# Kernel optimization log

Hardware: AMD Instinct MI355X
Metric: run time of the kernel (lower is better)

## Reference

```python
import jax, jax.numpy as jnp
import numpy as np

B, L, D = 8, 2048, 128
K_CURV = 1.0  # Lorentz manifold curvature constant
NEG_INF = float(-2**32 + 1)


def _lorentz_linear(x, W, b, scale):
    # nn.Linear then project onto the Lorentz manifold (dropout is identity in eval).
    x = x @ W.T + b
    time = jax.nn.sigmoid(x[..., :1]) * jnp.exp(scale) + 1.1
    x_narrow = x[..., 1:]
    s = (time * time - K_CURV) / jnp.sum(x_narrow * x_narrow, axis=-1, keepdims=True)
    return jnp.concatenate([time, x_narrow * jnp.sqrt(s)], axis=-1)


def setup_inputs() -> dict:
    key = jax.random.key(0)
    ks = jax.random.split(key, 10)
    stdv = 0.02

    def lin_w(k):
        W = jax.random.uniform(k, (D, D), minval=-stdv, maxval=stdv, dtype=jnp.float32)
        return W.at[:, 0].set(0.0)  # reset_parameters zeros column 0

    inp = {
        'query': jax.random.normal(ks[0], (B, L, D), dtype=jnp.float32),
        'key': jax.random.normal(ks[1], (B, L, D), dtype=jnp.float32),
        'value': jax.random.normal(ks[2], (B, L, D), dtype=jnp.float32),
        'mask': jax.random.bernoulli(ks[3], 0.1, (B, L)),  # True = padded position
        'Wq': lin_w(ks[4]), 'bq': jnp.zeros((D,), jnp.float32), 'sq': jnp.asarray(2.3, jnp.float32),
        'Wk': lin_w(ks[5]), 'bk': jnp.zeros((D,), jnp.float32), 'sk': jnp.asarray(2.3, jnp.float32),
        'Wv': lin_w(ks[6]), 'bv': jnp.zeros((D,), jnp.float32), 'sv': jnp.asarray(2.3, jnp.float32),
        'attn_scale': jnp.asarray([np.sqrt(D)], jnp.float32),
        'attn_bias': jnp.asarray(0.0, jnp.float32),
    }
    return inp


def reference(query, key, value, mask, Wq, bq, sq, Wk, bk, sk, Wv, bv, sv, attn_scale, attn_bias):
    q = _lorentz_linear(query, Wq, bq, sq)  # [B, L, D]
    k = _lorentz_linear(key, Wk, bk, sk)
    v = _lorentz_linear(value, Wv, bv, sv)
    # single head: shape to [B, 1, L, D]
    q, k, v = q[:, None], k[:, None], v[:, None]

    # Lorentzian inner product: negate time component of q
    qk = jnp.einsum('bhqd,bhkd->bhqk', q.at[..., 0].multiply(-1.0), k)
    attn = (2.0 + 2.0 * qk) / attn_scale + attn_bias  # [B, 1, L, L]

    # pad mask [B, L] broadcast over query rows + causal (triu) mask
    pad = jnp.broadcast_to(mask[:, None, :], (B, L, L))
    tri = jnp.triu(jnp.ones((L, L), bool), k=1)
    m = (tri[None] | pad)[:, None]  # [B, 1, L, L]
    attn = jnp.where(m, NEG_INF, attn)
    attn = jax.nn.softmax(attn, axis=-1)

    # Lorentz mid-point: weighted sum, normalize by sqrt(|<ave, ave>_L|)
    ave = jnp.einsum('bhqk,bhkd->bhqd', attn, v)
    lor = -ave[..., :1] ** 2 + jnp.sum(ave[..., 1:] ** 2, axis=-1, keepdims=True)
    denom = jnp.sqrt(jnp.maximum(jnp.abs(-lor), 1e-8))
    out = jnp.sqrt(K_CURV) * ave / denom
    return out[:, 0]  # [B, L, D]
```

## Files before the change

### kernel.cpp

```cpp
#include <hip/hip_runtime.h>

typedef unsigned short u16;
typedef unsigned long long u64;
typedef __attribute__((ext_vector_type(8))) short short8;
typedef __attribute__((ext_vector_type(4))) float f32x4;

#define MFMA16(A,B,C) __builtin_amdgcn_mfma_f32_16x16x32_bf16(A,B,C,0,0,0)
#define NEG_INF_F (-4294967295.0f)

#define Bsz 8
#define Lsz 2048
#define Dsz 128

__device__ __forceinline__ u16 f2bf(float f){
  union { float f; unsigned u; } v; v.f = f;
  unsigned u = v.u;
  return (u16)((u + 0x7fffu + ((u >> 16) & 1u)) >> 16);
}
__device__ __forceinline__ float bf2f(u16 h){
  union { float f; unsigned u; } v; v.u = ((unsigned)h) << 16;
  return v.f;
}

__global__ __launch_bounds__(256) void wconv_kernel(
    const float* __restrict__ Wq, const float* __restrict__ Wk,
    const float* __restrict__ Wv, u16* __restrict__ wb)
{
  int i = blockIdx.x * 256 + threadIdx.x;
  if (i < 16384) wb[i] = f2bf(Wq[i]);
  else if (i < 32768) wb[i] = f2bf(Wk[i - 16384]);
  else if (i < 49152) wb[i] = f2bf(Wv[i - 32768]);
}

#define LPX 136
#define LPY 133

__global__ __launch_bounds__(256) void proj_kernel(
    const float* __restrict__ xq, const float* __restrict__ xk, const float* __restrict__ xv,
    const u16* __restrict__ wb,
    const float* __restrict__ bq, const float* __restrict__ bk, const float* __restrict__ bv,
    const float* __restrict__ sq, const float* __restrict__ sk, const float* __restrict__ sv,
    const float* __restrict__ attn_scale,
    u16* __restrict__ qout, u16* __restrict__ kout,
    u16* __restrict__ vthi, u16* __restrict__ vtlo,
    float* __restrict__ tqo, float* __restrict__ tko,
    float* __restrict__ vpart)
{
  const int z = blockIdx.z;
  const float* x  = (z == 0) ? xq : (z == 1) ? xk : xv;
  const u16*   Wb = wb + z * 16384;
  const float* bb = (z == 0) ? bq : (z == 1) ? bk : bv;
  const float* ss = (z == 0) ? sq : (z == 1) ? sk : sv;

  __shared__ u16  xl[64 * LPX];
  __shared__ u16  wl[128 * LPX];
  __shared__ float yl[64 * LPY];
  __shared__ float scl[64];
  __shared__ float tml[64];

  const int t = threadIdx.x;
  const long row0 = (long)blockIdx.x * 64;

  for (int i = t; i < 2048; i += 256) {
    int r = i >> 4, c8 = (i & 15) * 8;
    *(short8*)&wl[r * LPX + c8] = *(const short8*)&Wb[r * 128 + c8];
  }
  for (int i = t; i < 2048; i += 256) {
    int off = i * 4;
    int r = off >> 7, c = off & 127;
    f32x4 xv4 = *(const f32x4*)(x + row0 * 128 + off);
    u64 wv = (u64)f2bf(xv4[0]) | ((u64)f2bf(xv4[1]) << 16)
           | ((u64)f2bf(xv4[2]) << 32) | ((u64)f2bf(xv4[3]) << 48);
    *(u64*)&xl[r * LPX + c] = wv;
  }
  __syncthreads();

  const int l = t & 63, wid = t >> 6;
  const int qr = l & 15, g = l >> 4;
  const int r0 = wid * 16;

  short8 af[4];
#pragma unroll
  for (int ks = 0; ks < 4; ks++)
    af[ks] = *(const short8*)&xl[(r0 + qr) * LPX + ks * 32 + g * 8];

  f32x4 acc[8];
#pragma unroll
  for (int jt = 0; jt < 8; jt++) acc[jt] = (f32x4){0.f, 0.f, 0.f, 0.f};

#pragma unroll
  for (int ks = 0; ks < 4; ks++) {
#pragma unroll
    for (int jt = 0; jt < 8; jt++) {
      short8 bfr = *(const short8*)&wl[(jt * 16 + qr) * LPX + ks * 32 + g * 8];
      acc[jt] = MFMA16(af[ks], bfr, acc[jt]);
    }
  }

  float bbv[8];
#pragma unroll
  for (int jt = 0; jt < 8; jt++) bbv[jt] = bb[jt * 16 + qr];

  float ssq[4] = {0.f, 0.f, 0.f, 0.f};
#pragma unroll
  for (int jt = 0; jt < 8; jt++)
#pragma unroll
    for (int r = 0; r < 4; r++) {
      float yv = acc[jt][r] + bbv[jt];
      acc[jt][r] = yv;
      float s2 = yv * yv;
      if (jt == 0) s2 = (qr == 0) ? 0.f : s2;
      ssq[r] += s2;
    }
#pragma unroll
  for (int r = 0; r < 4; r++) {
    ssq[r] += __shfl_xor(ssq[r], 1);
    ssq[r] += __shfl_xor(ssq[r], 2);
    ssq[r] += __shfl_xor(ssq[r], 4);
    ssq[r] += __shfl_xor(ssq[r], 8);
  }

  const float es = __expf(ss[0]);
  const float fold = 2.0f / attn_scale[0];

  float tvv[4], sclv[4];
#pragma unroll
  for (int r = 0; r < 4; r++) {
    float y0 = __shfl(acc[0][r], l & 48);
    float tv = es / (1.0f + __expf(-y0)) + 1.1f;
    tvv[r] = tv;
    sclv[r] = sqrtf((tv * tv - 1.0f) / ssq[r]);
  }
  if (qr == 0) {
#pragma unroll
    for (int r = 0; r < 4; r++) {
      tml[r0 + g * 4 + r] = tvv[r];
      scl[r0 + g * 4 + r] = sclv[r];
    }
  }
#pragma unroll
  for (int jt = 0; jt < 8; jt++)
#pragma unroll
    for (int r = 0; r < 4; r++)
      yl[(r0 + g * 4 + r) * LPY + jt * 16 + qr] = acc[jt][r];
  __syncthreads();

  const long gbase = row0 * 128;
  if (z == 0) {
    for (int i = t; i < 64 * 128; i += 256) {
      int r = i >> 7, d = i & 127;
      float v = (d == 0) ? 0.f : yl[r * LPY + d] * scl[r] * fold;
      qout[gbase + i] = f2bf(v);
    }
    if (t < 64) tqo[row0 + t] = -tml[t] * fold;
  } else if (z == 1) {
    for (int i = t; i < 64 * 128; i += 256) {
      int r = i >> 7, d = i & 127;
      float v = (d == 0) ? 0.f : yl[r * LPY + d] * scl[r];
      kout[gbase + i] = f2bf(v);
    }
    if (t < 64) tko[row0 + t] = tml[t];
  } else {
    const int b = (int)(row0 >> 11);
    const int lpos = (int)(row0 & 2047);
    for (int i = t; i < 128 * 64; i += 256) {
      int d = i >> 6, r = i & 63;
      float v = (d == 0) ? tml[r] : yl[r * LPY + d] * scl[r];
      u16 hi = f2bf(v);
      float lo = v - bf2f(hi);
      long idx = ((long)(b * 128 + d)) * 2048 + lpos + r;
      vthi[idx] = hi;
      vtlo[idx] = f2bf(lo);
    }
    if (t < 128) {
      float s = 0.f;
      for (int r = 0; r < 64; r++)
        s += (t == 0) ? tml[r] : yl[r * LPY + t] * scl[r];
      int blk = (int)((row0 >> 6) & 31);
      vpart[((long)(b * 32 + blk)) * 128 + t] = s;
    }
  }
}

__global__ __launch_bounds__(256) void pack_mask_kernel(
    const int* __restrict__ mask, u64* __restrict__ pmask)
{
  int gt = blockIdx.x * 256 + threadIdx.x;
  int w = gt >> 6;
  int lane = gt & 63;
  if (w >= Bsz * 32) return;
  u64 word = __ballot(mask[w * 64 + lane] != 0);
  if (lane == 0) pmask[w] = word;
}

__global__ __launch_bounds__(128) void vreduce_kernel(
    const float* __restrict__ vpart, float* __restrict__ vsum)
{
  int i = blockIdx.x * 128 + threadIdx.x;
  int b = i >> 7, d = i & 127;
  float s = 0.f;
  for (int j = 0; j < 32; j++) s += vpart[((long)(b * 32 + j)) * 128 + d];
  vsum[i] = s;
}

__global__ __launch_bounds__(512, 2) void flash_kernel(
    const u16* __restrict__ qbf, const u16* __restrict__ kb,
    const u16* __restrict__ vthi, const u16* __restrict__ vtlo,
    const float* __restrict__ tq, const float* __restrict__ tk,
    const u64* __restrict__ pmask, const float* __restrict__ vsum,
    const float* __restrict__ sqp, const float* __restrict__ skp,
    const float* __restrict__ asp,
    float* __restrict__ out)
{
  __shared__ u16 Pl[2][32 * 128];
  __shared__ float lLd[8][2][16];
  __shared__ float ssqw[8][2][16];

  const int t = threadIdx.x;
  const int w = t >> 6, l = t & 63;
  const int qr = l & 15, g = l >> 4;
  const int blk = blockIdx.x;
  const int b = blk & 7;
  const int s = 63 - (blk >> 3);
  const int qbase = s * 32;
  const int nkt = (qbase + 159) >> 7;

  const float fold = 2.0f / asp[0];
  const float tqm = __expf(sqp[0]) + 1.1f;
  const float tkm = __expf(skp[0]) + 1.1f;
  const float MS = fold * sqrtf((tqm * tqm - 1.f) * (tkm * tkm - 1.f)) + 1.0f;

  short8 qf[2][4];
  float tqv0, tqv1;
  {
    const u16* qp0 = qbf + ((long)(b * 2048 + qbase + qr)) * 128 + g * 8;
    const u16* qp1 = qp0 + 16 * 128;
#pragma unroll
    for (int ks = 0; ks < 4; ks++) {
      qf[0][ks] = *(const short8*)(qp0 + ks * 32);
      qf[1][ks] = *(const short8*)(qp1 + ks * 32);
    }
    tqv0 = tq[b * 2048 + qbase + qr];
    tqv1 = tq[b * 2048 + qbase + 16 + qr];
  }

  const u16* kbase  = kb   + ((long)(b * 2048 + 16 * w + qr)) * 128 + g * 8;
  const u16* vhbase = vthi + ((long)(b * 128 + 16 * w + qr)) * 2048 + g * 8;
  const u16* vlbase = vtlo + ((long)(b * 128 + 16 * w + qr)) * 2048 + g * 8;

  float lsum0 = 0.f, lsum1 = 0.f;
  f32x4 acc0 = (f32x4){0.f, 0.f, 0.f, 0.f};
  f32x4 acc1 = (f32x4){0.f, 0.f, 0.f, 0.f};

  short8 kc[4], vh[4], vl[4];
#pragma unroll
  for (int ks = 0; ks < 4; ks++) kc[ks] = *(const short8*)(kbase + ks * 32);
  f32x4 tkvc = *(const f32x4*)(tk + b * 2048 + 16 * w + g * 4);
  u64 mwc = pmask[b * 32 + (w >> 2)];

  int cur = 0;
  for (int kt = 0; kt < nkt; kt++) {
    const long k0 = (long)kt << 7;

    f32x4 sv0 = (f32x4){0.f, 0.f, 0.f, 0.f};
    f32x4 sv1 = (f32x4){0.f, 0.f, 0.f, 0.f};
#pragma unroll
    for (int ks = 0; ks < 4; ks++) {
      sv0 = MFMA16(kc[ks], qf[0][ks], sv0);
      sv1 = MFMA16(kc[ks], qf[1][ks], sv1);
    }
    if (kt + 1 < nkt) {
      const u16* kp = kbase + (k0 + 128) * 128;
#pragma unroll
      for (int ks = 0; ks < 4; ks++) kc[ks] = *(const short8*)(kp + ks * 32);
    }

    const bool bndry = (k0 + 127 > qbase);
    float p0[4], p1[4];
#pragma unroll
    for (int r = 0; r < 4; r++) {
      int kl = 16 * w + 4 * g + r;
      bool bad = ((mwc >> (kl & 63)) & 1ull) != 0ull;
      bool bad0 = bad, bad1 = bad;
      if (bndry) {
        bad0 |= (k0 + kl > qbase + qr);
        bad1 |= (k0 + kl > qbase + 16 + qr);
      }
      float e0 = __expf(sv0[r] + tqv0 * tkvc[r] - MS);
      float e1 = __expf(sv1[r] + tqv1 * tkvc[r] - MS);
      p0[r] = bad0 ? 0.f : e0;
      p1[r] = bad1 ? 0.f : e1;
      lsum0 += p0[r];
      lsum1 += p1[r];
    }
    {
      int pch = ((2 * w + (g >> 1)) ^ (qr & 7)) * 8 + (g & 1) * 4;
      u64 w0 = (u64)f2bf(p0[0]) | ((u64)f2bf(p0[1]) << 16)
             | ((u64)f2bf(p0[2]) << 32) | ((u64)f2bf(p0[3]) << 48);
      u64 w1 = (u64)f2bf(p1[0]) | ((u64)f2bf(p1[1]) << 16)
             | ((u64)f2bf(p1[2]) << 32) | ((u64)f2bf(p1[3]) << 48);
      *(u64*)&Pl[cur][qr * 128 + pch] = w0;
      *(u64*)&Pl[cur][(16 + qr) * 128 + pch] = w1;
    }
    if (kt + 1 < nkt) {
      tkvc = *(const f32x4*)(tk + b * 2048 + k0 + 128 + 16 * w + g * 4);
      mwc = pmask[b * 32 + (int)(k0 >> 6) + 2 + (w >> 2)];
    }

    if (kt > 0) {
      const u16* Pb = &Pl[cur ^ 1][0];
#pragma unroll
      for (int ks = 0; ks < 4; ks++) {
        int ch = ((4 * ks + g) ^ (qr & 7)) * 8;
        short8 pf0 = *(const short8*)&Pb[qr * 128 + ch];
        short8 pf1 = *(const short8*)&Pb[(16 + qr) * 128 + ch];
        acc0 = MFMA16(vh[ks], pf0, acc0);
        acc0 = MFMA16(vl[ks], pf0, acc0);
        acc1 = MFMA16(vh[ks], pf1, acc1);
        acc1 = MFMA16(vl[ks], pf1, acc1);
      }
    }

#pragma unroll
    for (int ks = 0; ks < 4; ks++) {
      vh[ks] = *(const short8*)(vhbase + k0 + ks * 32);
      vl[ks] = *(const short8*)(vlbase + k0 + ks * 32);
    }

    asm volatile("s_waitcnt lgkmcnt(0)\n\ts_barrier" ::: "memory");
    cur ^= 1;
  }

  {
    const u16* Pb = &Pl[cur ^ 1][0];
#pragma unroll
    for (int ks = 0; ks < 4; ks++) {
      int ch = ((4 * ks + g) ^ (qr & 7)) * 8;
      short8 pf0 = *(const short8*)&Pb[qr * 128 + ch];
      short8 pf1 = *(const short8*)&Pb[(16 + qr) * 128 + ch];
      acc0 = MFMA16(vh[ks], pf0, acc0);
      acc0 = MFMA16(vl[ks], pf0, acc0);
      acc1 = MFMA16(vh[ks], pf1, acc1);
      acc1 = MFMA16(vl[ks], pf1, acc1);
    }
  }

  lsum0 += __shfl_xor(lsum0, 16); lsum0 += __shfl_xor(lsum0, 32);
  lsum1 += __shfl_xor(lsum1, 16); lsum1 += __shfl_xor(lsum1, 32);
  if (g == 0) { lLd[w][0][qr] = lsum0; lLd[w][1][qr] = lsum1; }
  __syncthreads();

  float Lt0 = 0.f, Lt1 = 0.f;
#pragma unroll
  for (int j = 0; j < 8; j++) { Lt0 += lLd[j][0][qr]; Lt1 += lLd[j][1][qr]; }
  const bool mrow0 = (Lt0 == 0.f);
  const bool mrow1 = (Lt1 == 0.f);
  const float invL0 = mrow0 ? 0.f : 1.0f / Lt0;
  const float invL1 = mrow1 ? 0.f : 1.0f / Lt1;

  const float* vs = vsum + b * 128;
  float av0[4], av1[4];
  float pp0 = 0.f, pp1 = 0.f;
#pragma unroll
  for (int r = 0; r < 4; r++) {
    int d = 16 * w + 4 * g + r;
    float u = vs[d] * (1.0f / 2048.0f);
    float a0 = mrow0 ? u : acc0[r] * invL0;
    float a1 = mrow1 ? u : acc1[r] * invL1;
    av0[r] = a0; av1[r] = a1;
    float sgn = (d == 0) ? -1.f : 1.f;
    pp0 += sgn * a0 * a0;
    pp1 += sgn * a1 * a1;
  }
  pp0 += __shfl_xor(pp0, 16); pp0 += __shfl_xor(pp0, 32);
  pp1 += __shfl_xor(pp1, 16); pp1 += __shfl_xor(pp1, 32);
  if (g == 0) { ssqw[w][0][qr] = pp0; ssqw[w][1][qr] = pp1; }
  __syncthreads();

  float lor0 = 0.f, lor1 = 0.f;
#pragma unroll
  for (int j = 0; j < 8; j++) { lor0 += ssqw[j][0][qr]; lor1 += ssqw[j][1][qr]; }
  float rd0 = 1.0f / sqrtf(fmaxf(fabsf(lor0), 1e-8f));
  float rd1 = 1.0f / sqrtf(fmaxf(fabsf(lor1), 1e-8f));

  float* op0 = out + ((long)(b * 2048 + qbase + qr)) * 128 + 16 * w + 4 * g;
  float* op1 = out + ((long)(b * 2048 + qbase + 16 + qr)) * 128 + 16 * w + 4 * g;
  f32x4 o0, o1;
  o0[0] = av0[0] * rd0; o0[1] = av0[1] * rd0; o0[2] = av0[2] * rd0; o0[3] = av0[3] * rd0;
  o1[0] = av1[0] * rd1; o1[1] = av1[1] * rd1; o1[2] = av1[2] * rd1; o1[3] = av1[3] * rd1;
  *(f32x4*)op0 = o0;
  *(f32x4*)op1 = o1;
}

extern "C" void kernel_launch(void* const* d_in, const int* in_sizes, int n_in,
                              void* d_out, int out_size, void* d_ws, size_t ws_size,
                              hipStream_t stream)
{
  const float* query = (const float*)d_in[0];
  const float* key   = (const float*)d_in[1];
  const float* value = (const float*)d_in[2];
  const int*   mask  = (const int*)d_in[3];
  const float* Wq = (const float*)d_in[4];
  const float* bq = (const float*)d_in[5];
  const float* sq = (const float*)d_in[6];
  const float* Wk = (const float*)d_in[7];
  const float* bk = (const float*)d_in[8];
  const float* sk = (const float*)d_in[9];
  const float* Wv = (const float*)d_in[10];
  const float* bv = (const float*)d_in[11];
  const float* sv = (const float*)d_in[12];
  const float* attn_scale = (const float*)d_in[13];

  float* out = (float*)d_out;
  char* ws = (char*)d_ws;

  float* vsum  = (float*)ws;
  u64*   pmask = (u64*)(ws + 4096);
  float* tqa   = (float*)(ws + 8192);
  float* tka   = (float*)(ws + 8192 + 65536);
  float* vpart = (float*)(ws + 8192 + 131072);
  u16*   wb    = (u16*)(ws + 8192 + 262144);
  char*  big   = ws + 8192 + 262144 + 131072;
  u16*   qbuf  = (u16*)big;
  u16*   kbuf  = qbuf + (size_t)16384 * 128;
  u16*   vthi  = kbuf + (size_t)16384 * 128;
  u16*   vtlo  = vthi + (size_t)16384 * 128;

  wconv_kernel<<<192, 256, 0, stream>>>(Wq, Wk, Wv, wb);
  proj_kernel<<<dim3(256, 1, 3), 256, 0, stream>>>(
      query, key, value, wb, bq, bk, bv, sq, sk, sv, attn_scale,
      qbuf, kbuf, vthi, vtlo, tqa, tka, vpart);
  pack_mask_kernel<<<64, 256, 0, stream>>>(mask, pmask);
  vreduce_kernel<<<8, 128, 0, stream>>>(vpart, vsum);
  flash_kernel<<<512, 512, 0, stream>>>(
      qbuf, kbuf, vthi, vtlo, tqa, tka, pmask, vsum, sq, sk, attn_scale, out);
}
```

Baseline: 101.7 us.

## Enlarge flash query tile to 64 rows and fuse small prep kernels

The flash kernel now handles 64 query rows per block instead of 32, so each K and V fragment loaded from global memory feeds four MFMA row groups rather than two, and the grid is halved to 256 blocks. The weight bf16 conversion is folded into the projection kernel, and mask packing and the V-sum reduction are merged into one auxiliary kernel, cutting two launches. The trade-offs are higher register and LDS use per block, which can limit occupancy, and fewer blocks with coarser causal load balancing on a device with many CUs.

```diff
diff --git a/kernel.cpp b/kernel.cpp
--- a/kernel.cpp
+++ b/kernel.cpp
@@ -22,22 +22,12 @@
   return v.f;
 }
 
-__global__ __launch_bounds__(256) void wconv_kernel(
-    const float* __restrict__ Wq, const float* __restrict__ Wk,
-    const float* __restrict__ Wv, u16* __restrict__ wb)
-{
-  int i = blockIdx.x * 256 + threadIdx.x;
-  if (i < 16384) wb[i] = f2bf(Wq[i]);
-  else if (i < 32768) wb[i] = f2bf(Wk[i - 16384]);
-  else if (i < 49152) wb[i] = f2bf(Wv[i - 32768]);
-}
-
 #define LPX 136
 #define LPY 133
 
 __global__ __launch_bounds__(256) void proj_kernel(
     const float* __restrict__ xq, const float* __restrict__ xk, const float* __restrict__ xv,
-    const u16* __restrict__ wb,
+    const float* __restrict__ Wq, const float* __restrict__ Wk, const float* __restrict__ Wv,
     const float* __restrict__ bq, const float* __restrict__ bk, const float* __restrict__ bv,
     const float* __restrict__ sq, const float* __restrict__ sk, const float* __restrict__ sv,
     const float* __restrict__ attn_scale,
@@ -48,7 +38,7 @@
 {
   const int z = blockIdx.z;
   const float* x  = (z == 0) ? xq : (z == 1) ? xk : xv;
-  const u16*   Wb = wb + z * 16384;
+  const float* W  = (z == 0) ? Wq : (z == 1) ? Wk : Wv;
   const float* bb = (z == 0) ? bq : (z == 1) ? bk : bv;
   const float* ss = (z == 0) ? sq : (z == 1) ? sk : sv;
 
@@ -61,9 +51,13 @@
   const int t = threadIdx.x;
   const long row0 = (long)blockIdx.x * 64;
 
-  for (int i = t; i < 2048; i += 256) {
-    int r = i >> 4, c8 = (i & 15) * 8;
-    *(short8*)&wl[r * LPX + c8] = *(const short8*)&Wb[r * 128 + c8];
+  for (int i = t; i < 4096; i += 256) {
+    int off = i * 4;
+    int r = off >> 7, c = off & 127;
+    f32x4 wv4 = *(const f32x4*)(W + off);
+    u64 wv = (u64)f2bf(wv4[0]) | ((u64)f2bf(wv4[1]) << 16)
+           | ((u64)f2bf(wv4[2]) << 32) | ((u64)f2bf(wv4[3]) << 48);
+    *(u64*)&wl[r * LPX + c] = wv;
   }
   for (int i = t; i < 2048; i += 256) {
     int off = i * 4;
@@ -182,25 +176,24 @@
   }
 }
 
-__global__ __launch_bounds__(256) void pack_mask_kernel(
-    const int* __restrict__ mask, u64* __restrict__ pmask)
+__global__ __launch_bounds__(256) void aux_kernel(
+    const int* __restrict__ mask, u64* __restrict__ pmask,
+    const float* __restrict__ vpart, float* __restrict__ vsum)
 {
   int gt = blockIdx.x * 256 + threadIdx.x;
-  int w = gt >> 6;
+  int wword = gt >> 6;
   int lane = gt & 63;
-  if (w >= Bsz * 32) return;
-  u64 word = __ballot(mask[w * 64 + lane] != 0);
-  if (lane == 0) pmask[w] = word;
-}
-
-__global__ __launch_bounds__(128) void vreduce_kernel(
-    const float* __restrict__ vpart, float* __restrict__ vsum)
-{
-  int i = blockIdx.x * 128 + threadIdx.x;
-  int b = i >> 7, d = i & 127;
-  float s = 0.f;
-  for (int j = 0; j < 32; j++) s += vpart[((long)(b * 32 + j)) * 128 + d];
-  vsum[i] = s;
+  if (wword < Bsz * 32) {
+    u64 word = __ballot(mask[wword * 64 + lane] != 0);
+    if (lane == 0) pmask[wword] = word;
+  }
+  if (blockIdx.x < 4) {
+    int i = blockIdx.x * 256 + threadIdx.x;
+    int b = i >> 7, d = i & 127;
+    float s = 0.f;
+    for (int j = 0; j < 32; j++) s += vpart[((long)(b * 32 + j)) * 128 + d];
+    vsum[i] = s;
+  }
 }
 
 __global__ __launch_bounds__(512, 2) void flash_kernel(
@@ -212,45 +205,42 @@
     const float* __restrict__ asp,
     float* __restrict__ out)
 {
-  __shared__ u16 Pl[2][32 * 128];
-  __shared__ float lLd[8][2][16];
-  __shared__ float ssqw[8][2][16];
+  __shared__ u16 Pl[2][64 * 128];
+  __shared__ float lLd[8][4][16];
+  __shared__ float ssqw[8][4][16];
 
   const int t = threadIdx.x;
   const int w = t >> 6, l = t & 63;
   const int qr = l & 15, g = l >> 4;
   const int blk = blockIdx.x;
   const int b = blk & 7;
-  const int s = 63 - (blk >> 3);
-  const int qbase = s * 32;
-  const int nkt = (qbase + 159) >> 7;
+  const int s = 31 - (blk >> 3);
+  const int qbase = s * 64;
+  const int nkt = (qbase + 191) >> 7;
 
   const float fold = 2.0f / asp[0];
   const float tqm = __expf(sqp[0]) + 1.1f;
   const float tkm = __expf(skp[0]) + 1.1f;
   const float MS = fold * sqrtf((tqm * tqm - 1.f) * (tkm * tkm - 1.f)) + 1.0f;
 
-  short8 qf[2][4];
-  float tqv0, tqv1;
-  {
-    const u16* qp0 = qbf + ((long)(b * 2048 + qbase + qr)) * 128 + g * 8;
-    const u16* qp1 = qp0 + 16 * 128;
-#pragma unroll
-    for (int ks = 0; ks < 4; ks++) {
-      qf[0][ks] = *(const short8*)(qp0 + ks * 32);
-      qf[1][ks] = *(const short8*)(qp1 + ks * 32);
-    }
-    tqv0 = tq[b * 2048 + qbase + qr];
-    tqv1 = tq[b * 2048 + qbase + 16 + qr];
+  short8 qf[4][4];
+  float tqv[4];
+#pragma unroll
+  for (int qs = 0; qs < 4; qs++) {
+    const u16* qp = qbf + ((long)(b * 2048 + qbase + 16 * qs + qr)) * 128 + g * 8;
+#pragma unroll
+    for (int ks = 0; ks < 4; ks++) qf[qs][ks] = *(const short8*)(qp + ks * 32);
+    tqv[qs] = tq[b * 2048 + qbase + 16 * qs + qr];
   }
 
   const u16* kbase  = kb   + ((long)(b * 2048 + 16 * w + qr)) * 128 + g * 8;
   const u16* vhbase = vthi + ((long)(b * 128 + 16 * w + qr)) * 2048 + g * 8;
   const u16* vlbase = vtlo + ((long)(b * 128 + 16 * w + qr)) * 2048 + g * 8;
 
-  float lsum0 = 0.f, lsum1 = 0.f;
-  f32x4 acc0 = (f32x4){0.f, 0.f, 0.f, 0.f};
-  f32x4 acc1 = (f32x4){0.f, 0.f, 0.f, 0.f};
+  float lsum[4] = {0.f, 0.f, 0.f, 0.f};
+  f32x4 acc[4];
+#pragma unroll
+  for (int qs = 0; qs < 4; qs++) acc[qs] = (f32x4){0.f, 0.f, 0.f, 0.f};
 
   short8 kc[4], vh[4], vl[4];
 #pragma unroll
@@ -262,12 +252,14 @@
   for (int kt = 0; kt < nkt; kt++) {
     const long k0 = (long)kt << 7;
 
-    f32x4 sv0 = (f32x4){0.f, 0.f, 0.f, 0.f};
-    f32x4 sv1 = (f32x4){0.f, 0.f, 0.f, 0.f};
+    f32x4 sv[4];
+#pragma unroll
+    for (int qs = 0; qs < 4; qs++) sv[qs] = (f32x4){0.f, 0.f, 0.f, 0.f};
 #pragma unroll
     for (int ks = 0; ks < 4; ks++) {
-      sv0 = MFMA16(kc[ks], qf[0][ks], sv0);
-      sv1 = MFMA16(kc[ks], qf[1][ks], sv1);
+#pragma unroll
+      for (int qs = 0; qs < 4; qs++)
+        sv[qs] = MFMA16(kc[ks], qf[qs][ks], sv[qs]);
     }
     if (kt + 1 < nkt) {
       const u16* kp = kbase + (k0 + 128) * 128;
@@ -276,31 +268,22 @@
     }
 
     const bool bndry = (k0 + 127 > qbase);
-    float p0[4], p1[4];
-#pragma unroll
-    for (int r = 0; r < 4; r++) {
-      int kl = 16 * w + 4 * g + r;
-      bool bad = ((mwc >> (kl & 63)) & 1ull) != 0ull;
-      bool bad0 = bad, bad1 = bad;
-      if (bndry) {
-        bad0 |= (k0 + kl > qbase + qr);
-        bad1 |= (k0 + kl > qbase + 16 + qr);
+#pragma unroll
+    for (int qs = 0; qs < 4; qs++) {
+      float p4[4];
+#pragma unroll
+      for (int r = 0; r < 4; r++) {
+        int kl = 16 * w + 4 * g + r;
+        bool bad = ((mwc >> (kl & 63)) & 1ull) != 0ull;
+        if (bndry) bad |= (k0 + kl > qbase + 16 * qs + qr);
+        float e = __expf(sv[qs][r] + tqv[qs] * tkvc[r] - MS);
+        p4[r] = bad ? 0.f : e;
+        lsum[qs] += p4[r];
       }
-      float e0 = __expf(sv0[r] + tqv0 * tkvc[r] - MS);
-      float e1 = __expf(sv1[r] + tqv1 * tkvc[r] - MS);
-      p0[r] = bad0 ? 0.f : e0;
-      p1[r] = bad1 ? 0.f : e1;
-      lsum0 += p0[r];
-      lsum1 += p1[r];
-    }
-    {
       int pch = ((2 * w + (g >> 1)) ^ (qr & 7)) * 8 + (g & 1) * 4;
-      u64 w0 = (u64)f2bf(p0[0]) | ((u64)f2bf(p0[1]) << 16)
-             | ((u64)f2bf(p0[2]) << 32) | ((u64)f2bf(p0[3]) << 48);
-      u64 w1 = (u64)f2bf(p1[0]) | ((u64)f2bf(p1[1]) << 16)
-             | ((u64)f2bf(p1[2]) << 32) | ((u64)f2bf(p1[3]) << 48);
-      *(u64*)&Pl[cur][qr * 128 + pch] = w0;
-      *(u64*)&Pl[cur][(16 + qr) * 128 + pch] = w1;
+      u64 wv = (u64)f2bf(p4[0]) | ((u64)f2bf(p4[1]) << 16)
+             | ((u64)f2bf(p4[2]) << 32) | ((u64)f2bf(p4[3]) << 48);
+      *(u64*)&Pl[cur][(16 * qs + qr) * 128 + pch] = wv;
     }
     if (kt + 1 < nkt) {
       tkvc = *(const f32x4*)(tk + b * 2048 + k0 + 128 + 16 * w + g * 4);
@@ -312,12 +295,12 @@
 #pragma unroll
       for (int ks = 0; ks < 4; ks++) {
         int ch = ((4 * ks + g) ^ (qr & 7)) * 8;
-        short8 pf0 = *(const short8*)&Pb[qr * 128 + ch];
-        short8 pf1 = *(const short8*)&Pb[(16 + qr) * 128 + ch];
-        acc0 = MFMA16(vh[ks], pf0, acc0);
-        acc0 = MFMA16(vl[ks], pf0, acc0);
-        acc1 = MFMA16(vh[ks], pf1, acc1);
-        acc1 = MFMA16(vl[ks], pf1, acc1);
+#pragma unroll
+        for (int qs = 0; qs < 4; qs++) {
+          short8 pf = *(const short8*)&Pb[(16 * qs + qr) * 128 + ch];
+          acc[qs] = MFMA16(vh[ks], pf, acc[qs]);
+          acc[qs] = MFMA16(vl[ks], pf, acc[qs]);
+        }
       }
     }
 
@@ -336,60 +319,67 @@
 #pragma unroll
     for (int ks = 0; ks < 4; ks++) {
       int ch = ((4 * ks + g) ^ (qr & 7)) * 8;
-      short8 pf0 = *(const short8*)&Pb[qr * 128 + ch];
-      short8 pf1 = *(const short8*)&Pb[(16 + qr) * 128 + ch];
-      acc0 = MFMA16(vh[ks], pf0, acc0);
-      acc0 = MFMA16(vl[ks], pf0, acc0);
-      acc1 = MFMA16(vh[ks], pf1, acc1);
-      acc1 = MFMA16(vl[ks], pf1, acc1);
-    }
-  }
-
-  lsum0 += __shfl_xor(lsum0, 16); lsum0 += __shfl_xor(lsum0, 32);
-  lsum1 += __shfl_xor(lsum1, 16); lsum1 += __shfl_xor(lsum1, 32);
-  if (g == 0) { lLd[w][0][qr] = lsum0; lLd[w][1][qr] = lsum1; }
+#pragma unroll
+      for (int qs = 0; qs < 4; qs++) {
+        short8 pf = *(const short8*)&Pb[(16 * qs + qr) * 128 + ch];
+        acc[qs] = MFMA16(vh[ks], pf, acc[qs]);
+        acc[qs] = MFMA16(vl[ks], pf, acc[qs]);
+      }
+    }
+  }
+
+#pragma unroll
+  for (int qs = 0; qs < 4; qs++) {
+    lsum[qs] += __shfl_xor(lsum[qs], 16);
+    lsum[qs] += __shfl_xor(lsum[qs], 32);
+  }
+  if (g == 0) {
+#pragma unroll
+    for (int qs = 0; qs < 4; qs++) lLd[w][qs][qr] = lsum[qs];
+  }
   __syncthreads();
 
-  float Lt0 = 0.f, Lt1 = 0.f;
-#pragma unroll
-  for (int j = 0; j < 8; j++) { Lt0 += lLd[j][0][qr]; Lt1 += lLd[j][1][qr]; }
-  const bool mrow0 = (Lt0 == 0.f);
-  const bool mrow1 = (Lt1 == 0.f);
-  const float invL0 = mrow0 ? 0.f : 1.0f / Lt0;
-  const float invL1 = mrow1 ? 0.f : 1.0f / Lt1;
-
   const float* vs = vsum + b * 128;
-  float av0[4], av1[4];
-  float pp0 = 0.f, pp1 = 0.f;
-#pragma unroll
-  for (int r = 0; r < 4; r++) {
-    int d = 16 * w + 4 * g + r;
-    float u = vs[d] * (1.0f / 2048.0f);
-    float a0 = mrow0 ? u : acc0[r] * invL0;
-    float a1 = mrow1 ? u : acc1[r] * invL1;
-    av0[r] = a0; av1[r] = a1;
-    float sgn = (d == 0) ? -1.f : 1.f;
-    pp0 += sgn * a0 * a0;
-    pp1 += sgn * a1 * a1;
-  }
-  pp0 += __shfl_xor(pp0, 16); pp0 += __shfl_xor(pp0, 32);
-  pp1 += __shfl_xor(pp1, 16); pp1 += __shfl_xor(pp1, 32);
-  if (g == 0) { ssqw[w][0][qr] = pp0; ssqw[w][1][qr] = pp1; }
+  float av[4][4];
+  float pp[4] = {0.f, 0.f, 0.f, 0.f};
+#pragma unroll
+  for (int qs = 0; qs < 4; qs++) {
+    float Lt = 0.f;
+#pragma unroll
+    for (int j = 0; j < 8; j++) Lt += lLd[j][qs][qr];
+    const bool mrow = (Lt == 0.f);
+    const float invL = mrow ? 0.f : 1.0f / Lt;
+#pragma unroll
+    for (int r = 0; r < 4; r++) {
+      int d = 16 * w + 4 * g + r;
+      float u = vs[d] * (1.0f / 2048.0f);
+      float a = mrow ? u : acc[qs][r] * invL;
+      av[qs][r] = a;
+      float sgn = (d == 0) ? -1.f : 1.f;
+      pp[qs] += sgn * a * a;
+    }
+    pp[qs] += __shfl_xor(pp[qs], 16);
+    pp[qs] += __shfl_xor(pp[qs], 32);
+  }
+  if (g == 0) {
+#pragma unroll
+    for (int qs = 0; qs < 4; qs++) ssqw[w][qs][qr] = pp[qs];
+  }
   __syncthreads();
 
-  float lor0 = 0.f, lor1 = 0.f;
-#pragma unroll
-  for (int j = 0; j < 8; j++) { lor0 += ssqw[j][0][qr]; lor1 += ssqw[j][1][qr]; }
-  float rd0 = 1.0f / sqrtf(fmaxf(fabsf(lor0), 1e-8f));
-  float rd1 = 1.0f / sqrtf(fmaxf(fabsf(lor1), 1e-8f));
-
-  float* op0 = out + ((long)(b * 2048 + qbase + qr)) * 128 + 16 * w + 4 * g;
-  float* op1 = out + ((long)(b * 2048 + qbase + 16 + qr)) * 128 + 16 * w + 4 * g;
-  f32x4 o0, o1;
-  o0[0] = av0[0] * rd0; o0[1] = av0[1] * rd0; o0[2] = av0[2] * rd0; o0[3] = av0[3] * rd0;
-  o1[0] = av1[0] * rd1; o1[1] = av1[1] * rd1; o1[2] = av1[2] * rd1; o1[3] = av1[3] * rd1;
-  *(f32x4*)op0 = o0;
-  *(f32x4*)op1 = o1;
+#pragma unroll
+  for (int qs = 0; qs < 4; qs++) {
+    float lor = 0.f;
+#pragma unroll
+    for (int j = 0; j < 8; j++) lor += ssqw[j][qs][qr];
+    float rd = 1.0f / sqrtf(fmaxf(fabsf(lor), 1e-8f));
+    float* op = out + ((long)(b * 2048 + qbase + 16 * qs + qr)) * 128
+              + 16 * w + 4 * g;
+    f32x4 o;
+    o[0] = av[qs][0] * rd; o[1] = av[qs][1] * rd;
+    o[2] = av[qs][2] * rd; o[3] = av[qs][3] * rd;
+    *(f32x4*)op = o;
+  }
 }
 
 extern "C" void kernel_launch(void* const* d_in, const int* in_sizes, int n_in,
@@ -419,19 +409,16 @@
   float* tqa   = (float*)(ws + 8192);
   float* tka   = (float*)(ws + 8192 + 65536);
   float* vpart = (float*)(ws + 8192 + 131072);
-  u16*   wb    = (u16*)(ws + 8192 + 262144);
-  char*  big   = ws + 8192 + 262144 + 131072;
+  char*  big   = ws + 8192 + 262144;
   u16*   qbuf  = (u16*)big;
   u16*   kbuf  = qbuf + (size_t)16384 * 128;
   u16*   vthi  = kbuf + (size_t)16384 * 128;
   u16*   vtlo  = vthi + (size_t)16384 * 128;
 
-  wconv_kernel<<<192, 256, 0, stream>>>(Wq, Wk, Wv, wb);
   proj_kernel<<<dim3(256, 1, 3), 256, 0, stream>>>(
-      query, key, value, wb, bq, bk, bv, sq, sk, sv, attn_scale,
+      query, key, value, Wq, Wk, Wv, bq, bk, bv, sq, sk, sv, attn_scale,
       qbuf, kbuf, vthi, vtlo, tqa, tka, vpart);
-  pack_mask_kernel<<<64, 256, 0, stream>>>(mask, pmask);
-  vreduce_kernel<<<8, 128, 0, stream>>>(vpart, vsum);
-  flash_kernel<<<512, 512, 0, stream>>>(
+  aux_kernel<<<64, 256, 0, stream>>>(mask, pmask, vpart, vsum);
+  flash_kernel<<<256, 512, 0, stream>>>(
       qbuf, kbuf, vthi, vtlo, tqa, tka, pmask, vsum, sq, sk, attn_scale, out);
 }
```

Result: slower. 108.1 us (+6.4%).
